# Kernel tuning notes

Hardware: AMD Instinct MI355X
Metric: run time of the kernel (lower is better)

## Reference

```python
import jax, jax.numpy as jnp
import numpy as np

LN_EPS = 1e-5


def setup_inputs() -> dict:
    key = jax.random.key(0)
    k1, = jax.random.split(key, 1)
    B, C, H, W = 16, 512, 64, 64
    HW = H * W
    x = jax.random.normal(k1, (B, C, H, W), dtype=jnp.float32)
    gamma = jnp.ones((), dtype=jnp.float32)          # Scale(1) learnable scalar
    ln_weight = jnp.ones((HW,), dtype=jnp.float32)   # LayerNorm weight
    ln_bias = jnp.zeros((HW,), dtype=jnp.float32)    # LayerNorm bias
    return {"x": x, "gamma": gamma, "ln_weight": ln_weight, "ln_bias": ln_bias}


def reference(x, gamma, ln_weight, ln_bias):
    B, C, H, W = x.shape
    v = x.reshape(B, C, H * W)                       # [B, C, HW] (Q = K = V)
    energy = jnp.einsum('bcn,bdn->bcd', v, v)        # [B, C, C]
    attn = jax.nn.softmax(energy, axis=-1)
    out = jnp.einsum('bcd,bdn->bcn', attn, v)        # [B, C, HW]
    out = gamma * out + v                            # scale + residual
    # LayerNorm over last dim (HW), torch eps=1e-5
    mean = jnp.mean(out, axis=-1, keepdims=True)
    var = jnp.mean(jnp.square(out - mean), axis=-1, keepdims=True)
    out = (out - mean) * jax.lax.rsqrt(var + LN_EPS) * ln_weight + ln_bias
    return out.reshape(B, C, H, W)
```

## Files before the change

kernel.cpp:

```cpp
#include <hip/hip_runtime.h>
#include <hip/hip_bf16.h>

#define B_DIM 16
#define C_DIM 512
#define HW_DIM 4096
#define LN_EPS 1e-5f
#define ATTN_STRIDE 1024

using bf16 = __hip_bfloat16;
typedef __bf16 v8bf __attribute__((ext_vector_type(8)));
typedef float v4f __attribute__((ext_vector_type(4)));
typedef unsigned short v8us __attribute__((ext_vector_type(8)));
typedef unsigned short v4us __attribute__((ext_vector_type(4)));
using gptr_t = const __attribute__((address_space(1))) void*;
using lptr_t = __attribute__((address_space(3))) void*;

__device__ __forceinline__ unsigned short f2bf(float f) {
  unsigned int u = __float_as_uint(f);
  u = (u + 0x7fffu + ((u >> 16) & 1u)) >> 16;
  return (unsigned short)u;
}
__device__ __forceinline__ float bf2f(unsigned short us) {
  return __uint_as_float(((unsigned int)us) << 16);
}

__global__ __launch_bounds__(256) void k_convert(
    const float* __restrict__ x, unsigned short* __restrict__ v) {
  const size_t i0 = ((size_t)blockIdx.x * 256 + threadIdx.x) * 8;
  const size_t step = (size_t)2048 * 256 * 8;
#pragma unroll
  for (int it = 0; it < 8; ++it) {
    const size_t base = i0 + (size_t)it * step;
    const float4 f0 = ((const float4*)(x + base))[0];
    const float4 f1 = ((const float4*)(x + base))[1];
    v8us pack;
    pack[0] = f2bf(f0.x); pack[1] = f2bf(f0.y);
    pack[2] = f2bf(f0.z); pack[3] = f2bf(f0.w);
    pack[4] = f2bf(f1.x); pack[5] = f2bf(f1.y);
    pack[6] = f2bf(f1.z); pack[7] = f2bf(f1.w);
    *(v8us*)(v + base) = pack;
  }
}

__global__ __launch_bounds__(256) void k_transpose(
    const unsigned short* __restrict__ v, unsigned short* __restrict__ vt) {
  __shared__ unsigned short tile[64 * 64];
  const int tid = threadIdx.x;
  const int b = blockIdx.z;
  const int n0 = blockIdx.x * 64;
  const int c0 = blockIdx.y * 64;
  const size_t boff = (size_t)b * ((size_t)C_DIM * HW_DIM);
  const unsigned short* vb = v + boff;
  unsigned short* vtb = vt + boff;

  const int cl = tid >> 3;
  const int hb = tid & 7;
#pragma unroll
  for (int j = 0; j < 2; ++j) {
    const int c = cl + j * 32;
    const v8us pack = *(const v8us*)(vb + (size_t)(c0 + c) * HW_DIM + n0 + hb * 8);
    const int key = (c & 7) ^ ((c >> 3) & 7);
    *(v8us*)(tile + c * 64 + ((hb ^ key) << 3)) = pack;
  }
  __syncthreads();
  const int nl = tid >> 3;
  const int c8 = (tid & 7) * 8;
  const int n = 2 * nl;
  v8us pa, pb;
#pragma unroll
  for (int e = 0; e < 8; ++e) {
    const int r = c8 + e;
    const int key = (r & 7) ^ ((r >> 3) & 7);
    const unsigned int w = *(const unsigned int*)(
        tile + r * 64 + (((n >> 3) ^ key) << 3) + (n & 7));
    pa[e] = (unsigned short)(w & 0xffffu);
    pb[e] = (unsigned short)(w >> 16);
  }
  *(v8us*)(vtb + (size_t)(n0 + n) * C_DIM + c0 + c8) = pa;
  *(v8us*)(vtb + (size_t)(n0 + n + 1) * C_DIM + c0 + c8) = pb;
}

#define TILE_E (256 * 64)

__device__ __forceinline__ void stage_half8(
    const bf16* __restrict__ g, bf16* l, int k0, int stride, int wave, int lane) {
  const int lrow = lane >> 3, lc = lane & 7;
#pragma unroll
  for (int i = 0; i < 2; ++i) {
    const int row = i * 64 + wave * 8 + lrow;
    __builtin_amdgcn_global_load_lds(
        (gptr_t)(g + (size_t)row * stride + k0 + ((lc ^ (row & 7)) << 3)),
        (lptr_t)(l + (i * 64 + wave * 8) * 64), 16, 0, 0);
  }
}
__device__ __forceinline__ void stage_op2(
    const bf16* __restrict__ g, bf16* l, int k0, int stride, int wave, int lane) {
  stage_half8(g, l, k0, stride, wave, lane);
  stage_half8(g + (size_t)128 * stride, l + 128 * 64, k0, stride, wave, lane);
}
__device__ __forceinline__ v8bf ld_frag8(const bf16* l, int row, int j) {
  return *(const v8bf*)(l + row * 64 + ((j ^ (row & 7)) << 3));
}

__device__ __forceinline__ void gemm_8ph_loop(
    const bf16* __restrict__ Ab, const bf16* __restrict__ Bb,
    const int strideA, const int strideB, const int kts,
    bf16* smem, const int wave, const int lane, v4f acc[8][4]) {
  const int wm = wave >> 2, wn = wave & 3;
  const int rl = lane & 15, kq = lane >> 4;

  stage_op2(Bb, smem + 2 * TILE_E, 0, strideB, wave, lane);
  stage_op2(Ab, smem, 0, strideA, wave, lane);
  stage_op2(Bb, smem + 3 * TILE_E, 64, strideB, wave, lane);
  stage_op2(Ab, smem + TILE_E, 64, strideA, wave, lane);
  asm volatile("s_waitcnt vmcnt(8)" ::: "memory");
  __builtin_amdgcn_s_barrier();

  v8bf a[4][2], b01[2][2], b23[2][2];
  for (int kt = 0; kt < kts; ++kt) {
    const bf16* LA = smem + (kt & 1) * TILE_E;
    const bf16* LB = smem + (2 + (kt & 1)) * TILE_E;
    bf16* SA = smem + (kt & 1) * TILE_E;
    bf16* SB = smem + (2 + (kt & 1)) * TILE_E;
#pragma unroll
    for (int mi = 0; mi < 4; ++mi)
#pragma unroll
      for (int kk = 0; kk < 2; ++kk)
        a[mi][kk] = ld_frag8(LA, wm * 128 + mi * 16 + rl, kk * 4 + kq);
#pragma unroll
    for (int ni = 0; ni < 2; ++ni)
#pragma unroll
      for (int kk = 0; kk < 2; ++kk)
        b01[ni][kk] = ld_frag8(LB, wn * 64 + ni * 16 + rl, kk * 4 + kq);
    __builtin_amdgcn_s_barrier();
    asm volatile("s_waitcnt lgkmcnt(0)");
    __builtin_amdgcn_s_setprio(1);
#pragma unroll
    for (int kk = 0; kk < 2; ++kk)
#pragma unroll
      for (int mi = 0; mi < 4; ++mi)
#pragma unroll
        for (int ni = 0; ni < 2; ++ni)
          acc[mi][ni] = __builtin_amdgcn_mfma_f32_16x16x32_bf16(
              a[mi][kk], b01[ni][kk], acc[mi][ni], 0, 0, 0);
    __builtin_amdgcn_s_setprio(0);
    __builtin_amdgcn_s_barrier();
#pragma unroll
    for (int ni = 0; ni < 2; ++ni)
#pragma unroll
      for (int kk = 0; kk < 2; ++kk)
        b23[ni][kk] = ld_frag8(LB, wn * 64 + (ni + 2) * 16 + rl, kk * 4 + kq);
    __builtin_amdgcn_s_barrier();
    asm volatile("s_waitcnt lgkmcnt(0)");
    __builtin_amdgcn_s_setprio(1);
#pragma unroll
    for (int kk = 0; kk < 2; ++kk)
#pragma unroll
      for (int mi = 0; mi < 4; ++mi)
#pragma unroll
        for (int ni = 0; ni < 2; ++ni)
          acc[mi][ni + 2] = __builtin_amdgcn_mfma_f32_16x16x32_bf16(
              a[mi][kk], b23[ni][kk], acc[mi][ni + 2], 0, 0, 0);
    __builtin_amdgcn_s_setprio(0);
    __builtin_amdgcn_s_barrier();
#pragma unroll
    for (int mi = 0; mi < 4; ++mi)
#pragma unroll
      for (int kk = 0; kk < 2; ++kk)
        a[mi][kk] = ld_frag8(LA, wm * 128 + (mi + 4) * 16 + rl, kk * 4 + kq);
    if (kt < kts - 2) stage_op2(Bb, SB, (kt + 2) * 64, strideB, wave, lane);
    __builtin_amdgcn_s_barrier();
    asm volatile("s_waitcnt lgkmcnt(0)");
    __builtin_amdgcn_s_setprio(1);
#pragma unroll
    for (int kk = 0; kk < 2; ++kk)
#pragma unroll
      for (int mi = 0; mi < 4; ++mi)
#pragma unroll
        for (int ni = 0; ni < 2; ++ni)
          acc[mi + 4][ni + 2] = __builtin_amdgcn_mfma_f32_16x16x32_bf16(
              a[mi][kk], b23[ni][kk], acc[mi + 4][ni + 2], 0, 0, 0);
    __builtin_amdgcn_s_setprio(0);
    __builtin_amdgcn_s_barrier();
    if (kt < kts - 2) stage_op2(Ab, SA, (kt + 2) * 64, strideA, wave, lane);
    __builtin_amdgcn_s_barrier();
    __builtin_amdgcn_s_setprio(1);
#pragma unroll
    for (int kk = 0; kk < 2; ++kk)
#pragma unroll
      for (int mi = 0; mi < 4; ++mi)
#pragma unroll
        for (int ni = 0; ni < 2; ++ni)
          acc[mi + 4][ni] = __builtin_amdgcn_mfma_f32_16x16x32_bf16(
              a[mi][kk], b01[ni][kk], acc[mi + 4][ni], 0, 0, 0);
    __builtin_amdgcn_s_setprio(0);
    if (kt < kts - 2)
      asm volatile("s_waitcnt vmcnt(8)" ::: "memory");
    else if (kt == kts - 2)
      asm volatile("s_waitcnt vmcnt(0)" ::: "memory");
    __builtin_amdgcn_s_barrier();
  }
}

__device__ __forceinline__ void epilogue_bounce(
    v4f acc[8][4], bf16* smem, float* ob, const int out_stride,
    const int wave, const int lane) {
  const int wm = wave >> 2, wn = wave & 3;
  const int rl = lane & 15, kq = lane >> 4;
  float* smf = (float*)smem;
#pragma unroll
  for (int h = 0; h < 2; ++h) {
    if (wm == h) {
#pragma unroll
      for (int mi = 0; mi < 8; ++mi)
#pragma unroll
        for (int ni = 0; ni < 4; ++ni)
#pragma unroll
          for (int rr = 0; rr < 4; ++rr) {
            const int rloc = mi * 16 + kq * 4 + rr;
            const int col = wn * 64 + ni * 16 + rl;
            const int key = rloc & 7;
            smf[rloc * 256 + ((((col >> 2) ^ key) << 2) | (col & 3))] =
                acc[mi][ni][rr];
          }
    }
    __syncthreads();
#pragma unroll
    for (int it = 0; it < 16; ++it) {
      const int rloc = it * 8 + wave;
      const float4 vv =
          *(const float4*)(smf + rloc * 256 + ((lane ^ (rloc & 7)) << 2));
      *(float4*)(ob + (size_t)(h * 128 + rloc) * out_stride + lane * 4) = vv;
    }
    __syncthreads();
  }
}

__global__ __launch_bounds__(512, 2) void k_gemm1(
    const bf16* __restrict__ v, float* __restrict__ e_part) {
  __shared__ __align__(16) bf16 smem[4 * TILE_E];
  const int bid = blockIdx.x;
  const int t = (bid & 7) * 32 + (bid >> 3);
  const int ks = t & 3;
  const int db = (t >> 2) & 1;
  const int cb = (t >> 3) & 1;
  const int b = t >> 4;
  const int tid = threadIdx.x;
  const int wave = tid >> 6, lane = tid & 63;

  const bf16* vb = v + (size_t)b * ((size_t)C_DIM * HW_DIM) + ks * 1024;
  const bf16* Ab = vb + (size_t)(cb * 256) * HW_DIM;
  const bf16* Bb = vb + (size_t)(db * 256) * HW_DIM;

  v4f acc[8][4] = {};
  gemm_8ph_loop(Ab, Bb, HW_DIM, HW_DIM, 16, smem, wave, lane, acc);

  float* ob = e_part + (size_t)ks * ((size_t)B_DIM * C_DIM * C_DIM) +
              (size_t)b * (C_DIM * C_DIM) + (size_t)(cb * 256) * C_DIM + db * 256;
  epilogue_bounce(acc, smem, ob, C_DIM, wave, lane);
}

__global__ __launch_bounds__(256) void k_softmax(
    const float* __restrict__ e_part, unsigned short* __restrict__ attn) {
  const int row = blockIdx.x;
  const size_t bcc = (size_t)B_DIM * C_DIM * C_DIM;
  const float* e0 = e_part + (size_t)row * C_DIM;
  const int tid = threadIdx.x;
  float v0 = 0.f, v1 = 0.f;
#pragma unroll
  for (int p = 0; p < 4; ++p) {
    v0 += e0[p * bcc + tid];
    v1 += e0[p * bcc + tid + 256];
  }
  float mx = fmaxf(v0, v1);
#pragma unroll
  for (int off = 32; off > 0; off >>= 1) mx = fmaxf(mx, __shfl_xor(mx, off));
  __shared__ float rmax[4], rsum[4];
  const int wv = tid >> 6, ln = tid & 63;
  if (ln == 0) rmax[wv] = mx;
  __syncthreads();
  mx = fmaxf(fmaxf(rmax[0], rmax[1]), fmaxf(rmax[2], rmax[3]));
  const float p0 = __expf(v0 - mx), p1 = __expf(v1 - mx);
  float s = p0 + p1;
#pragma unroll
  for (int off = 32; off > 0; off >>= 1) s += __shfl_xor(s, off);
  if (ln == 0) rsum[wv] = s;
  __syncthreads();
  s = rsum[0] + rsum[1] + rsum[2] + rsum[3];
  const float inv = 1.0f / s;
  attn[(size_t)row * ATTN_STRIDE + tid] = f2bf(p0 * inv);
  attn[(size_t)row * ATTN_STRIDE + tid + 256] = f2bf(p1 * inv);
}

__global__ __launch_bounds__(512, 2) void k_gemm2(
    const bf16* __restrict__ attn, const bf16* __restrict__ vt,
    float* __restrict__ out) {
  __shared__ __align__(16) bf16 smem[4 * TILE_E];
  const int bid = blockIdx.x;
  const int t = (bid & 7) * 64 + (bid >> 3);
  const int b = t >> 5;
  const int cb = (t >> 4) & 1;
  const int nb = t & 15;
  const int tid = threadIdx.x;
  const int wave = tid >> 6, lane = tid & 63;

  const bf16* Ab = attn + (size_t)(b * C_DIM + cb * 256) * ATTN_STRIDE;
  const bf16* Bb = vt + (size_t)b * ((size_t)C_DIM * HW_DIM) +
                   (size_t)(nb * 256) * C_DIM;

  v4f acc[8][4] = {};
  gemm_8ph_loop(Ab, Bb, ATTN_STRIDE, C_DIM, 8, smem, wave, lane, acc);

  float* ob = out + (size_t)b * ((size_t)C_DIM * HW_DIM) +
              (size_t)(cb * 256) * HW_DIM + nb * 256;
  epilogue_bounce(acc, smem, ob, HW_DIM, wave, lane);
}

__global__ __launch_bounds__(256) void k_ln(
    float* __restrict__ out, const unsigned short* __restrict__ vres,
    const float* __restrict__ gamma, const float* __restrict__ w,
    const float* __restrict__ bias) {
  const int row = blockIdx.x;
  float* p = out + (size_t)row * HW_DIM;
  const unsigned short* vr = vres + (size_t)row * HW_DIM;
  const float g = gamma[0];
  const int tid = threadIdx.x;
  float4 vals[4];
  float s = 0.f, ss = 0.f;
#pragma unroll
  for (int i = 0; i < 4; ++i) {
    const int idx = tid + i * 256;
    const float4 av = ((const float4*)p)[idx];
    const v4us rv = *(const v4us*)(vr + idx * 4);
    float4 vv;
    vv.x = g * av.x + bf2f(rv[0]);
    vv.y = g * av.y + bf2f(rv[1]);
    vv.z = g * av.z + bf2f(rv[2]);
    vv.w = g * av.w + bf2f(rv[3]);
    vals[i] = vv;
    s += vv.x + vv.y + vv.z + vv.w;
    ss += vv.x * vv.x + vv.y * vv.y + vv.z * vv.z + vv.w * vv.w;
  }
#pragma unroll
  for (int off = 32; off > 0; off >>= 1) {
    s += __shfl_xor(s, off);
    ss += __shfl_xor(ss, off);
  }
  __shared__ float rs[4], rss[4];
  const int wv = tid >> 6, ln = tid & 63;
  if (ln == 0) { rs[wv] = s; rss[wv] = ss; }
  __syncthreads();
  s = rs[0] + rs[1] + rs[2] + rs[3];
  ss = rss[0] + rss[1] + rss[2] + rss[3];
  const float mean = s * (1.f / HW_DIM);
  const float var = ss * (1.f / HW_DIM) - mean * mean;
  const float rstd = rsqrtf(var + LN_EPS);
#pragma unroll
  for (int i = 0; i < 4; ++i) {
    const int idx = tid + i * 256;
    const float4 vv = vals[i];
    const float4 w4 = ((const float4*)w)[idx];
    const float4 b4 = ((const float4*)bias)[idx];
    float4 r;
    r.x = (vv.x - mean) * rstd * w4.x + b4.x;
    r.y = (vv.y - mean) * rstd * w4.y + b4.y;
    r.z = (vv.z - mean) * rstd * w4.z + b4.z;
    r.w = (vv.w - mean) * rstd * w4.w + b4.w;
    ((float4*)p)[idx] = r;
  }
}

extern "C" void kernel_launch(void* const* d_in, const int* in_sizes, int n_in,
                              void* d_out, int out_size, void* d_ws, size_t ws_size,
                              hipStream_t stream) {
  const float* x = (const float*)d_in[0];
  const float* gamma = (const float*)d_in[1];
  const float* lnw = (const float*)d_in[2];
  const float* lnb = (const float*)d_in[3];
  float* out = (float*)d_out;
  char* ws = (char*)d_ws;

  const size_t n_elem = (size_t)B_DIM * C_DIM * HW_DIM;
  unsigned short* vbf = (unsigned short*)ws;
  unsigned short* vbfT = (unsigned short*)(ws + 2 * n_elem);
  float* e_part = (float*)(ws + 4 * n_elem);
  unsigned short* attn = (unsigned short*)e_part;

  k_convert<<<2048, 256, 0, stream>>>(x, vbf);
  k_transpose<<<dim3(HW_DIM / 64, C_DIM / 64, B_DIM), 256, 0, stream>>>(
      vbf, vbfT);
  k_gemm1<<<256, 512, 0, stream>>>((const bf16*)vbf, e_part);
  k_softmax<<<B_DIM * C_DIM, 256, 0, stream>>>(e_part, attn);
  k_gemm2<<<512, 512, 0, stream>>>((const bf16*)attn, (const bf16*)vbfT, out);
  k_ln<<<B_DIM * C_DIM, 256, 0, stream>>>(out, vbf, gamma, lnw, lnb);
}
```

Measured before the change: 238.1 us.

## Fuse V transpose into gemm2 by register-transposing B tiles into LDS

Removes the standalone transpose kernel and its transposed bf16 copy of V. In gemm2, half the threads load row-major V tiles into registers, transpose them in-register and write them swizzled into LDS, prefetching two k-tiles ahead. The other half stage the attention operand with direct global-to-LDS loads. This saves a full read/write pass over V and one launch, but adds register pressure and LDS write work inside the GEMM main loop.

```diff
diff --git a/kernel.cpp b/kernel.cpp
--- a/kernel.cpp
+++ b/kernel.cpp
@@ -42,44 +42,6 @@
   }
 }
 
-__global__ __launch_bounds__(256) void k_transpose(
-    const unsigned short* __restrict__ v, unsigned short* __restrict__ vt) {
-  __shared__ unsigned short tile[64 * 64];
-  const int tid = threadIdx.x;
-  const int b = blockIdx.z;
-  const int n0 = blockIdx.x * 64;
-  const int c0 = blockIdx.y * 64;
-  const size_t boff = (size_t)b * ((size_t)C_DIM * HW_DIM);
-  const unsigned short* vb = v + boff;
-  unsigned short* vtb = vt + boff;
-
-  const int cl = tid >> 3;
-  const int hb = tid & 7;
-#pragma unroll
-  for (int j = 0; j < 2; ++j) {
-    const int c = cl + j * 32;
-    const v8us pack = *(const v8us*)(vb + (size_t)(c0 + c) * HW_DIM + n0 + hb * 8);
-    const int key = (c & 7) ^ ((c >> 3) & 7);
-    *(v8us*)(tile + c * 64 + ((hb ^ key) << 3)) = pack;
-  }
-  __syncthreads();
-  const int nl = tid >> 3;
-  const int c8 = (tid & 7) * 8;
-  const int n = 2 * nl;
-  v8us pa, pb;
-#pragma unroll
-  for (int e = 0; e < 8; ++e) {
-    const int r = c8 + e;
-    const int key = (r & 7) ^ ((r >> 3) & 7);
-    const unsigned int w = *(const unsigned int*)(
-        tile + r * 64 + (((n >> 3) ^ key) << 3) + (n & 7));
-    pa[e] = (unsigned short)(w & 0xffffu);
-    pb[e] = (unsigned short)(w >> 16);
-  }
-  *(v8us*)(vtb + (size_t)(n0 + n) * C_DIM + c0 + c8) = pa;
-  *(v8us*)(vtb + (size_t)(n0 + n + 1) * C_DIM + c0 + c8) = pb;
-}
-
 #define TILE_E (256 * 64)
 
 __device__ __forceinline__ void stage_half8(
@@ -100,6 +62,34 @@
 }
 __device__ __forceinline__ v8bf ld_frag8(const bf16* l, int row, int j) {
   return *(const v8bf*)(l + row * 64 + ((j ^ (row & 7)) << 3));
+}
+__device__ __forceinline__ v8bf ld_frag8B(const bf16* l, int row, int j) {
+  const int key = (row & 7) ^ ((row >> 3) & 7);
+  return *(const v8bf*)(l + row * 64 + ((j ^ key) << 3));
+}
+__device__ __forceinline__ void stageA8(
+    const bf16* __restrict__ g, bf16* l, int k0, int stride,
+    int w4, int lrow, int lc) {
+#pragma unroll
+  for (int i = 0; i < 8; ++i) {
+    const int row = i * 32 + w4 * 8 + lrow;
+    __builtin_amdgcn_global_load_lds(
+        (gptr_t)(g + (size_t)row * stride + k0 + ((lc ^ (row & 7)) << 3)),
+        (lptr_t)(l + (i * 32 + w4 * 8) * 64), 16, 0, 0);
+  }
+}
+__device__ __forceinline__ void bwrite8(
+    bf16* lb, const v8us bu[8], int dblk, int n8) {
+  unsigned short* lu = (unsigned short*)lb;
+#pragma unroll
+  for (int j = 0; j < 8; ++j) {
+    const int n = n8 + j;
+    const int key = (n & 7) ^ ((n >> 3) & 7);
+    v8us p;
+#pragma unroll
+    for (int r = 0; r < 8; ++r) p[r] = bu[r][j];
+    *(v8us*)(lu + n * 64 + ((dblk ^ key) << 3)) = p;
+  }
 }
 
 __device__ __forceinline__ void gemm_8ph_loop(
@@ -293,7 +283,7 @@
 }
 
 __global__ __launch_bounds__(512, 2) void k_gemm2(
-    const bf16* __restrict__ attn, const bf16* __restrict__ vt,
+    const bf16* __restrict__ attn, const bf16* __restrict__ v,
     float* __restrict__ out) {
   __shared__ __align__(16) bf16 smem[4 * TILE_E];
   const int bid = blockIdx.x;
@@ -303,13 +293,131 @@
   const int nb = t & 15;
   const int tid = threadIdx.x;
   const int wave = tid >> 6, lane = tid & 63;
+  const int rl = lane & 15, kq = lane >> 4;
+  const int wm = wave >> 2, wn = wave & 3;
 
   const bf16* Ab = attn + (size_t)(b * C_DIM + cb * 256) * ATTN_STRIDE;
-  const bf16* Bb = vt + (size_t)b * ((size_t)C_DIM * HW_DIM) +
-                   (size_t)(nb * 256) * C_DIM;
+  const bf16* Vb = v + (size_t)b * ((size_t)C_DIM * HW_DIM) + nb * 256;
+
+  const bool isB = (tid < 256);
+  const int w4 = wave & 3;
+  const int lrow = lane >> 3, lc = lane & 7;
+  const int dblk = (tid & 255) >> 5;
+  const int n8 = (tid & 31) * 8;
 
   v4f acc[8][4] = {};
-  gemm_8ph_loop(Ab, Bb, ATTN_STRIDE, C_DIM, 8, smem, wave, lane, acc);
+  v8us bu[8];
+
+  if (isB) {
+#pragma unroll
+    for (int r = 0; r < 8; ++r)
+      bu[r] = *(const v8us*)((const unsigned short*)Vb +
+                             (size_t)(dblk * 8 + r) * HW_DIM + n8);
+    bwrite8(smem + 2 * TILE_E, bu, dblk, n8);
+#pragma unroll
+    for (int r = 0; r < 8; ++r)
+      bu[r] = *(const v8us*)((const unsigned short*)Vb +
+                             (size_t)(64 + dblk * 8 + r) * HW_DIM + n8);
+    bwrite8(smem + 3 * TILE_E, bu, dblk, n8);
+  } else {
+    stageA8(Ab, smem, 0, ATTN_STRIDE, w4, lrow, lc);
+    stageA8(Ab, smem + TILE_E, 64, ATTN_STRIDE, w4, lrow, lc);
+  }
+  asm volatile("s_waitcnt vmcnt(8)" ::: "memory");
+  __builtin_amdgcn_s_barrier();
+
+  v8bf a[4][2], b01[2][2], b23[2][2];
+  for (int kt = 0; kt < 8; ++kt) {
+    const bf16* LA = smem + (kt & 1) * TILE_E;
+    const bf16* LB = smem + (2 + (kt & 1)) * TILE_E;
+    bf16* SA = smem + (kt & 1) * TILE_E;
+    bf16* SB = smem + (2 + (kt & 1)) * TILE_E;
+#pragma unroll
+    for (int mi = 0; mi < 4; ++mi)
+#pragma unroll
+      for (int kk = 0; kk < 2; ++kk)
+        a[mi][kk] = ld_frag8(LA, wm * 128 + mi * 16 + rl, kk * 4 + kq);
+#pragma unroll
+    for (int ni = 0; ni < 2; ++ni)
+#pragma unroll
+      for (int kk = 0; kk < 2; ++kk)
+        b01[ni][kk] = ld_frag8B(LB, wn * 64 + ni * 16 + rl, kk * 4 + kq);
+    if (isB && kt < 6) {
+      const int d0 = (kt + 2) * 64 + dblk * 8;
+#pragma unroll
+      for (int r = 0; r < 8; ++r)
+        bu[r] = *(const v8us*)((const unsigned short*)Vb +
+                               (size_t)(d0 + r) * HW_DIM + n8);
+    }
+    __builtin_amdgcn_s_barrier();
+    asm volatile("s_waitcnt lgkmcnt(0)");
+    __builtin_amdgcn_s_setprio(1);
+#pragma unroll
+    for (int kk = 0; kk < 2; ++kk)
+#pragma unroll
+      for (int mi = 0; mi < 4; ++mi)
+#pragma unroll
+        for (int ni = 0; ni < 2; ++ni)
+          acc[mi][ni] = __builtin_amdgcn_mfma_f32_16x16x32_bf16(
+              a[mi][kk], b01[ni][kk], acc[mi][ni], 0, 0, 0);
+    __builtin_amdgcn_s_setprio(0);
+    __builtin_amdgcn_s_barrier();
+#pragma unroll
+    for (int ni = 0; ni < 2; ++ni)
+#pragma unroll
+      for (int kk = 0; kk < 2; ++kk)
+        b23[ni][kk] = ld_frag8B(LB, wn * 64 + (ni + 2) * 16 + rl, kk * 4 + kq);
+    __builtin_amdgcn_s_barrier();
+    asm volatile("s_waitcnt lgkmcnt(0)");
+    __builtin_amdgcn_s_setprio(1);
+#pragma unroll
+    for (int kk = 0; kk < 2; ++kk)
+#pragma unroll
+      for (int mi = 0; mi < 4; ++mi)
+#pragma unroll
+        for (int ni = 0; ni < 2; ++ni)
+          acc[mi][ni + 2] = __builtin_amdgcn_mfma_f32_16x16x32_bf16(
+              a[mi][kk], b23[ni][kk], acc[mi][ni + 2], 0, 0, 0);
+    __builtin_amdgcn_s_setprio(0);
+    __builtin_amdgcn_s_barrier();
+#pragma unroll
+    for (int mi = 0; mi < 4; ++mi)
+#pragma unroll
+      for (int kk = 0; kk < 2; ++kk)
+        a[mi][kk] = ld_frag8(LA, wm * 128 + (mi + 4) * 16 + rl, kk * 4 + kq);
+    if (isB && kt < 6) bwrite8(SB, bu, dblk, n8);
+    __builtin_amdgcn_s_barrier();
+    asm volatile("s_waitcnt lgkmcnt(0)");
+    __builtin_amdgcn_s_setprio(1);
+#pragma unroll
+    for (int kk = 0; kk < 2; ++kk)
+#pragma unroll
+      for (int mi = 0; mi < 4; ++mi)
+#pragma unroll
+        for (int ni = 0; ni < 2; ++ni)
+          acc[mi + 4][ni + 2] = __builtin_amdgcn_mfma_f32_16x16x32_bf16(
+              a[mi][kk], b23[ni][kk], acc[mi + 4][ni + 2], 0, 0, 0);
+    __builtin_amdgcn_s_setprio(0);
+    __builtin_amdgcn_s_barrier();
+    if (!isB && kt < 6)
+      stageA8(Ab, SA, (kt + 2) * 64, ATTN_STRIDE, w4, lrow, lc);
+    __builtin_amdgcn_s_barrier();
+    __builtin_amdgcn_s_setprio(1);
+#pragma unroll
+    for (int kk = 0; kk < 2; ++kk)
+#pragma unroll
+      for (int mi = 0; mi < 4; ++mi)
+#pragma unroll
+        for (int ni = 0; ni < 2; ++ni)
+          acc[mi + 4][ni] = __builtin_amdgcn_mfma_f32_16x16x32_bf16(
+              a[mi][kk], b01[ni][kk], acc[mi + 4][ni], 0, 0, 0);
+    __builtin_amdgcn_s_setprio(0);
+    if (kt < 6)
+      asm volatile("s_waitcnt vmcnt(8)" ::: "memory");
+    else if (kt == 6)
+      asm volatile("s_waitcnt vmcnt(0)" ::: "memory");
+    __builtin_amdgcn_s_barrier();
+  }
 
   float* ob = out + (size_t)b * ((size_t)C_DIM * HW_DIM) +
               (size_t)(cb * 256) * HW_DIM + nb * 256;
@@ -382,15 +490,12 @@
 
   const size_t n_elem = (size_t)B_DIM * C_DIM * HW_DIM;
   unsigned short* vbf = (unsigned short*)ws;
-  unsigned short* vbfT = (unsigned short*)(ws + 2 * n_elem);
   float* e_part = (float*)(ws + 4 * n_elem);
   unsigned short* attn = (unsigned short*)e_part;
 
   k_convert<<<2048, 256, 0, stream>>>(x, vbf);
-  k_transpose<<<dim3(HW_DIM / 64, C_DIM / 64, B_DIM), 256, 0, stream>>>(
-      vbf, vbfT);
   k_gemm1<<<256, 512, 0, stream>>>((const bf16*)vbf, e_part);
   k_softmax<<<B_DIM * C_DIM, 256, 0, stream>>>(e_part, attn);
-  k_gemm2<<<512, 512, 0, stream>>>((const bf16*)attn, (const bf16*)vbfT, out);
+  k_gemm2<<<512, 512, 0, stream>>>((const bf16*)attn, (const bf16*)vbf, out);
   k_ln<<<B_DIM * C_DIM, 256, 0, stream>>>(out, vbf, gamma, lnw, lnb);
 }
```

Measured after the change: 243.4 us. 1.02x slower.
